# Kernel tuning notes

Hardware: AMD Instinct MI355X
Metric: run time of the kernel (lower is better)

The kernel has to match this reference:

```python
import jax, jax.numpy as jnp
import numpy as np

N_NODES = 100000
N_EDGES = 1600000
D_IN = 256
D_OUT = 256


def setup_inputs() -> dict:
    key = jax.random.key(0)
    k1, k2, k3, k4, k5 = jax.random.split(key, 5)
    x = jax.random.normal(k1, (N_NODES, D_IN), dtype=jnp.float32)
    edge_src = jax.random.randint(k2, (N_EDGES,), 0, N_NODES, dtype=jnp.int32)
    edge_dst = jax.random.randint(k3, (N_EDGES,), 0, N_NODES, dtype=jnp.int32)
    edge_val = jax.random.uniform(k4, (N_EDGES,), dtype=jnp.float32)
    stdv = 1.0 / np.sqrt(D_OUT)
    weight = jax.random.uniform(k5, (D_IN, D_OUT), dtype=jnp.float32,
                                minval=-stdv, maxval=stdv)
    return {"x": x, "edge_src": edge_src, "edge_dst": edge_dst,
            "edge_val": edge_val, "weight": weight}


def reference(x, edge_src, edge_dst, edge_val, weight):
    # torch.spmm(adj, x): out[dst] += adj_val * x[src]
    msgs = x[edge_src] * edge_val[:, None]                     # [E, D_IN]
    agg = jax.ops.segment_sum(msgs, edge_dst,
                              num_segments=x.shape[0])         # [N, D_IN]
    # torch.mm(aggregated, weight)
    return agg @ weight                                        # [N, D_OUT]
```

## Files before the change

kernel.cpp:

```cpp
#include <hip/hip_runtime.h>
#include <hip/hip_bf16.h>

#define D 256
#define BDST 128
#define CAP 3072
#define TILE 6144

typedef __attribute__((ext_vector_type(8))) short short8;
typedef __attribute__((ext_vector_type(4))) float f32x4;

static __device__ __forceinline__ unsigned short f2bf(float f) {
    union { float f; unsigned u; } u; u.f = f;
    unsigned r = u.u + 0x7FFF + ((u.u >> 16) & 1);
    return (unsigned short)(r >> 16);
}

static __device__ __forceinline__ float bf2f(unsigned short b) {
    union { unsigned u; float f; } u; u.u = ((unsigned)b) << 16;
    return u.f;
}

static __device__ __forceinline__ unsigned cvtpk(float a, float b) {
    unsigned r;
    asm("v_cvt_pk_bf16_f32 %0, %1, %2" : "=v"(r) : "v"(a), "v"(b));
    return r;
}

__global__ __launch_bounds__(64) void build_wf_kernel(
    const float* __restrict__ W, unsigned short* __restrict__ wF) {
    int fid = blockIdx.x;
    int kt = fid >> 4, nt = fid & 15;
    int lane = threadIdx.x;
    int col = nt * 16 + (lane & 15);
    int k0 = kt * 32 + (lane >> 4) * 8;
    unsigned short frag[8];
#pragma unroll
    for (int j = 0; j < 8; ++j) frag[j] = f2bf(W[(k0 + j) * D + col]);
    *(short8*)(wF + ((size_t)fid * 64 + lane) * 8) = *(short8*)frag;
}

__global__ __launch_bounds__(256) void gemm_kernel(
    const float* __restrict__ x, const unsigned short* __restrict__ wF,
    unsigned short* __restrict__ y, int n_nodes) {
    const int lane = threadIdx.x & 63;
    const int wave = threadIdx.x >> 6;
    const int rsel = lane & 15;
    const int koff = (lane >> 4) * 8;
    const int row0 = blockIdx.x * 64 + wave * 16;
    if (row0 >= n_nodes) return;

    int row = row0 + rsel;
    int rowc = row < n_nodes ? row : n_nodes - 1;
    const float* xp = x + (size_t)rowc * D + koff;

    short8 a[8];
#pragma unroll
    for (int kt = 0; kt < 8; ++kt) {
        f32x4 lo = *(const f32x4*)(xp + kt * 32);
        f32x4 hi = *(const f32x4*)(xp + kt * 32 + 4);
        union { unsigned u[4]; short8 s; } pk;
        pk.u[0] = cvtpk(lo[0], lo[1]);
        pk.u[1] = cvtpk(lo[2], lo[3]);
        pk.u[2] = cvtpk(hi[0], hi[1]);
        pk.u[3] = cvtpk(hi[2], hi[3]);
        a[kt] = pk.s;
    }

    f32x4 acc[16];
#pragma unroll
    for (int nt = 0; nt < 16; ++nt) acc[nt] = (f32x4){0.f, 0.f, 0.f, 0.f};

    const short8* wf = (const short8*)wF;
#pragma unroll
    for (int kt = 0; kt < 8; ++kt) {
#pragma unroll
        for (int nt = 0; nt < 16; ++nt) {
            short8 b = wf[(kt * 16 + nt) * 64 + lane];
            acc[nt] = __builtin_amdgcn_mfma_f32_16x16x32_bf16(a[kt], b, acc[nt], 0, 0, 0);
        }
    }

    int crow0 = row0 + (lane >> 4) * 4;
#pragma unroll
    for (int nt = 0; nt < 16; ++nt) {
        int ccol = nt * 16 + rsel;
#pragma unroll
        for (int i = 0; i < 4; ++i) {
            int r = crow0 + i;
            if (r < n_nodes) y[(size_t)r * D + ccol] = f2bf(acc[nt][i]);
        }
    }
}

__global__ __launch_bounds__(256) void hist_bucket_kernel(
    const int* __restrict__ edst, int* __restrict__ gcount,
    int n_edges, int nb) {
    __shared__ int h[1024];
    for (int j = threadIdx.x; j < nb; j += 256) h[j] = 0;
    __syncthreads();
    int i = blockIdx.x * 256 + threadIdx.x;
    int stride = gridDim.x * 256;
    for (; i < n_edges; i += stride) atomicAdd(&h[edst[i] >> 7], 1);
    __syncthreads();
    for (int j = threadIdx.x; j < nb; j += 256) {
        int v = h[j];
        if (v) atomicAdd(&gcount[j], v);
    }
}

__global__ __launch_bounds__(1024) void scan_bucket_kernel(
    const int* __restrict__ gcount, int* __restrict__ offs,
    int* __restrict__ cursor, int nb) {
    __shared__ int t[1024];
    int tid = threadIdx.x;
    int c = (tid < nb) ? gcount[tid] : 0;
    t[tid] = c;
    __syncthreads();
    for (int off = 1; off < 1024; off <<= 1) {
        int v = (tid >= off) ? t[tid - off] : 0;
        __syncthreads();
        t[tid] += v;
        __syncthreads();
    }
    if (tid < nb) { int e = t[tid] - c; offs[tid] = e; cursor[tid] = e; }
}

__global__ __launch_bounds__(1024) void fill_ms_kernel(
    const int* __restrict__ esrc, const int* __restrict__ edst,
    const float* __restrict__ eval, int* __restrict__ cursor,
    int2* __restrict__ binned, int n_edges, int nb) {
    __shared__ int lhist[1024];
    __shared__ int lscan[1024];
    __shared__ int lbase[1024];
    __shared__ int lcur[1024];

    int tid = threadIdx.x;
    int tb = blockIdx.x * TILE;
    int m = n_edges - tb; if (m > TILE) m = TILE;

    int src[6], dst[6]; float val[6];
#pragma unroll
    for (int j = 0; j < 6; ++j) {
        int i = tid + j * 1024;
        if (i < m) { src[j] = esrc[tb + i]; dst[j] = edst[tb + i]; val[j] = eval[tb + i]; }
    }

    for (int j = tid; j < nb; j += 1024) lhist[j] = 0;
    __syncthreads();
#pragma unroll
    for (int j = 0; j < 6; ++j)
        if (tid + j * 1024 < m) atomicAdd(&lhist[dst[j] >> 7], 1);
    __syncthreads();

    int c = (tid < nb) ? lhist[tid] : 0;
    lscan[tid] = c;
    __syncthreads();
    for (int off = 1; off < 1024; off <<= 1) {
        int v = (tid >= off) ? lscan[tid - off] : 0;
        __syncthreads();
        lscan[tid] += v;
        __syncthreads();
    }
    if (tid < nb) {
        int lofs = lscan[tid] - c;
        int gbase = c ? atomicAdd(&cursor[tid], c) : 0;
        lbase[tid] = gbase - lofs;
        lcur[tid] = lofs;
    }
    __syncthreads();

#pragma unroll
    for (int j = 0; j < 6; ++j) {
        if (tid + j * 1024 < m) {
            int d = dst[j];
            int b = d >> 7;
            int pos = atomicAdd(&lcur[b], 1);
            binned[lbase[b] + pos] =
                make_int2(src[j] | ((d & (BDST - 1)) << 20), __float_as_int(val[j]));
        }
    }
}

__global__ __launch_bounds__(512) void bucket_gather_kernel(
    const unsigned short* __restrict__ y, const int* __restrict__ offs,
    const int* __restrict__ bend, const int2* __restrict__ binned,
    float* __restrict__ out, int n_nodes) {
    __shared__ int2 lcsr[CAP];
    __shared__ int lhist[BDST];
    __shared__ int lscan[BDST];
    __shared__ int lofs[BDST];
    __shared__ int lcur[BDST];

    int b = blockIdx.x;
    int tid = threadIdx.x;
    int beg = offs[b];
    int end = bend[b];
    int cnt = end - beg;
    int nch = cnt > 0 ? (cnt + CAP - 1) / CAP : 1;

    const int hw = tid >> 5;
    const int lane = tid & 31;
    const unsigned short* yl = y + lane * 8;

    for (int c = 0; c < nch; ++c) {
        int cb = beg + c * CAP;
        int ce = cb + CAP < end ? cb + CAP : end;
        int m = ce > cb ? ce - cb : 0;

        int2 ec[6];
#pragma unroll
        for (int j = 0; j < 6; ++j) {
            int i = tid + j * 512;
            if (i < m) ec[j] = binned[cb + i];
        }

        for (int j = tid; j < BDST; j += 512) lhist[j] = 0;
        __syncthreads();
#pragma unroll
        for (int j = 0; j < 6; ++j)
            if (tid + j * 512 < m) atomicAdd(&lhist[(ec[j].x >> 20) & (BDST - 1)], 1);
        __syncthreads();
        if (tid < BDST) lscan[tid] = lhist[tid];
        __syncthreads();
        for (int off = 1; off < BDST; off <<= 1) {
            int v = 0;
            if (tid < BDST && tid >= off) v = lscan[tid - off];
            __syncthreads();
            if (tid < BDST) lscan[tid] += v;
            __syncthreads();
        }
        if (tid < BDST) {
            int e = lscan[tid] - lhist[tid];
            lofs[tid] = e;
            lcur[tid] = e;
        }
        __syncthreads();
#pragma unroll
        for (int j = 0; j < 6; ++j) {
            if (tid + j * 512 < m) {
                int pos = atomicAdd(&lcur[(ec[j].x >> 20) & (BDST - 1)], 1);
                lcsr[pos] = ec[j];
            }
        }
        __syncthreads();

        for (int dl = hw; dl < BDST; dl += 16) {
            int d = b * BDST + dl;
            if (d >= n_nodes) break;
            int i0 = lofs[dl];
            int i1 = lcur[dl];
            float acc[8] = {0.f, 0.f, 0.f, 0.f, 0.f, 0.f, 0.f, 0.f};
            int i = i0;
            for (; i + 4 <= i1; i += 4) {
                int2 e0 = lcsr[i];
                int2 e1 = lcsr[i + 1];
                int2 e2 = lcsr[i + 2];
                int2 e3 = lcsr[i + 3];
                short8 r0 = *(const short8*)(yl + (size_t)(e0.x & 0xFFFFF) * D);
                short8 r1 = *(const short8*)(yl + (size_t)(e1.x & 0xFFFFF) * D);
                short8 r2 = *(const short8*)(yl + (size_t)(e2.x & 0xFFFFF) * D);
                short8 r3 = *(const short8*)(yl + (size_t)(e3.x & 0xFFFFF) * D);
                float v0 = __int_as_float(e0.y), v1 = __int_as_float(e1.y);
                float v2 = __int_as_float(e2.y), v3 = __int_as_float(e3.y);
#pragma unroll
                for (int j = 0; j < 8; ++j) {
                    acc[j] += v0 * bf2f((unsigned short)r0[j]);
                    acc[j] += v1 * bf2f((unsigned short)r1[j]);
                    acc[j] += v2 * bf2f((unsigned short)r2[j]);
                    acc[j] += v3 * bf2f((unsigned short)r3[j]);
                }
            }
            for (; i < i1; ++i) {
                int2 e0 = lcsr[i];
                float v0 = __int_as_float(e0.y);
                short8 r0 = *(const short8*)(yl + (size_t)(e0.x & 0xFFFFF) * D);
#pragma unroll
                for (int j = 0; j < 8; ++j) acc[j] += v0 * bf2f((unsigned short)r0[j]);
            }
            float* op = out + (size_t)d * D + lane * 8;
            if (c == 0) {
                *(f32x4*)(op)     = (f32x4){acc[0], acc[1], acc[2], acc[3]};
                *(f32x4*)(op + 4) = (f32x4){acc[4], acc[5], acc[6], acc[7]};
            } else {
                f32x4 o0 = *(f32x4*)(op);
                f32x4 o1 = *(f32x4*)(op + 4);
                o0[0] += acc[0]; o0[1] += acc[1]; o0[2] += acc[2]; o0[3] += acc[3];
                o1[0] += acc[4]; o1[1] += acc[5]; o1[2] += acc[6]; o1[3] += acc[7];
                *(f32x4*)(op)     = o0;
                *(f32x4*)(op + 4) = o1;
            }
        }
        __syncthreads();
    }
}

extern "C" void kernel_launch(void* const* d_in, const int* in_sizes, int n_in,
                              void* d_out, int out_size, void* d_ws, size_t ws_size,
                              hipStream_t stream) {
    const float* x    = (const float*)d_in[0];
    const int*   esrc = (const int*)d_in[1];
    const int*   edst = (const int*)d_in[2];
    const float* eval = (const float*)d_in[3];
    const float* W    = (const float*)d_in[4];
    float* out = (float*)d_out;

    const int n_nodes = in_sizes[0] / D;
    const int n_edges = in_sizes[1];
    const int nb = (n_nodes + BDST - 1) / BDST;

    char* ws = (char*)d_ws;
    unsigned short* y  = (unsigned short*)ws;  ws += (size_t)n_nodes * D * 2;
    unsigned short* wF = (unsigned short*)ws;  ws += (size_t)D * D * 2;
    int*  gcount  = (int*)ws;                  ws += 4096;
    int*  offs    = (int*)ws;                  ws += 4096;
    int*  cursor  = (int*)ws;                  ws += 4096;
    int2* binned  = (int2*)ws;                 ws += (size_t)n_edges * 8;

    hipMemsetAsync(gcount, 0, (size_t)nb * sizeof(int), stream);

    build_wf_kernel<<<128, 64, 0, stream>>>(W, wF);
    gemm_kernel<<<(n_nodes + 63) / 64, 256, 0, stream>>>(x, wF, y, n_nodes);

    hist_bucket_kernel<<<256, 256, 0, stream>>>(edst, gcount, n_edges, nb);
    scan_bucket_kernel<<<1, 1024, 0, stream>>>(gcount, offs, cursor, nb);

    const int ntiles = (n_edges + TILE - 1) / TILE;
    fill_ms_kernel<<<ntiles, 1024, 0, stream>>>(esrc, edst, eval, cursor, binned, n_edges, nb);

    bucket_gather_kernel<<<nb, 512, 0, stream>>>(y, offs, cursor, binned, out, n_nodes);
}
```

Measured before the change: 244.5 us.

## Merge GEMM with edge binning and weight prep with histogram into shared launches

The weight fragment build is folded into the edge histogram kernel, and the dense GEMM is merged with the edge binning fill kernel. Block-index ranges pick the role, so the memory-bound binning and the MFMA GEMM can run at the same time on the GPU, with fewer launches. The fill tile shrinks to 256-thread blocks, each thread scanning 4 buckets. The gather kernel moves to 256 threads with a smaller per-chunk edge capacity. The costs are more global cursor atomics from the smaller fill tiles and fewer waves per gather block.

```diff
diff --git a/kernel.cpp b/kernel.cpp
--- a/kernel.cpp
+++ b/kernel.cpp
@@ -3,8 +3,8 @@
 
 #define D 256
 #define BDST 128
-#define CAP 3072
-#define TILE 6144
+#define CAP 2560
+#define TILE 2048
 
 typedef __attribute__((ext_vector_type(8))) short short8;
 typedef __attribute__((ext_vector_type(4))) float f32x4;
@@ -26,85 +26,33 @@
     return r;
 }
 
-__global__ __launch_bounds__(64) void build_wf_kernel(
-    const float* __restrict__ W, unsigned short* __restrict__ wF) {
-    int fid = blockIdx.x;
-    int kt = fid >> 4, nt = fid & 15;
-    int lane = threadIdx.x;
-    int col = nt * 16 + (lane & 15);
-    int k0 = kt * 32 + (lane >> 4) * 8;
-    unsigned short frag[8];
-#pragma unroll
-    for (int j = 0; j < 8; ++j) frag[j] = f2bf(W[(k0 + j) * D + col]);
-    *(short8*)(wF + ((size_t)fid * 64 + lane) * 8) = *(short8*)frag;
-}
-
-__global__ __launch_bounds__(256) void gemm_kernel(
-    const float* __restrict__ x, const unsigned short* __restrict__ wF,
-    unsigned short* __restrict__ y, int n_nodes) {
-    const int lane = threadIdx.x & 63;
-    const int wave = threadIdx.x >> 6;
-    const int rsel = lane & 15;
-    const int koff = (lane >> 4) * 8;
-    const int row0 = blockIdx.x * 64 + wave * 16;
-    if (row0 >= n_nodes) return;
-
-    int row = row0 + rsel;
-    int rowc = row < n_nodes ? row : n_nodes - 1;
-    const float* xp = x + (size_t)rowc * D + koff;
-
-    short8 a[8];
-#pragma unroll
-    for (int kt = 0; kt < 8; ++kt) {
-        f32x4 lo = *(const f32x4*)(xp + kt * 32);
-        f32x4 hi = *(const f32x4*)(xp + kt * 32 + 4);
-        union { unsigned u[4]; short8 s; } pk;
-        pk.u[0] = cvtpk(lo[0], lo[1]);
-        pk.u[1] = cvtpk(lo[2], lo[3]);
-        pk.u[2] = cvtpk(hi[0], hi[1]);
-        pk.u[3] = cvtpk(hi[2], hi[3]);
-        a[kt] = pk.s;
-    }
-
-    f32x4 acc[16];
-#pragma unroll
-    for (int nt = 0; nt < 16; ++nt) acc[nt] = (f32x4){0.f, 0.f, 0.f, 0.f};
-
-    const short8* wf = (const short8*)wF;
-#pragma unroll
-    for (int kt = 0; kt < 8; ++kt) {
-#pragma unroll
-        for (int nt = 0; nt < 16; ++nt) {
-            short8 b = wf[(kt * 16 + nt) * 64 + lane];
-            acc[nt] = __builtin_amdgcn_mfma_f32_16x16x32_bf16(a[kt], b, acc[nt], 0, 0, 0);
-        }
-    }
-
-    int crow0 = row0 + (lane >> 4) * 4;
-#pragma unroll
-    for (int nt = 0; nt < 16; ++nt) {
-        int ccol = nt * 16 + rsel;
-#pragma unroll
-        for (int i = 0; i < 4; ++i) {
-            int r = crow0 + i;
-            if (r < n_nodes) y[(size_t)r * D + ccol] = f2bf(acc[nt][i]);
-        }
-    }
-}
-
-__global__ __launch_bounds__(256) void hist_bucket_kernel(
+__global__ __launch_bounds__(256) void prep_kernel(
+    const float* __restrict__ W, unsigned short* __restrict__ wF,
     const int* __restrict__ edst, int* __restrict__ gcount,
     int n_edges, int nb) {
-    __shared__ int h[1024];
-    for (int j = threadIdx.x; j < nb; j += 256) h[j] = 0;
-    __syncthreads();
-    int i = blockIdx.x * 256 + threadIdx.x;
-    int stride = gridDim.x * 256;
-    for (; i < n_edges; i += stride) atomicAdd(&h[edst[i] >> 7], 1);
-    __syncthreads();
-    for (int j = threadIdx.x; j < nb; j += 256) {
-        int v = h[j];
-        if (v) atomicAdd(&gcount[j], v);
+    int tid = threadIdx.x;
+    if (blockIdx.x < 32) {
+        int fid = blockIdx.x * 4 + (tid >> 6);
+        int lane = tid & 63;
+        int kt = fid >> 4, nt = fid & 15;
+        int col = nt * 16 + (lane & 15);
+        int k0 = kt * 32 + (lane >> 4) * 8;
+        unsigned short frag[8];
+#pragma unroll
+        for (int j = 0; j < 8; ++j) frag[j] = f2bf(W[(k0 + j) * D + col]);
+        *(short8*)(wF + ((size_t)fid * 64 + lane) * 8) = *(short8*)frag;
+    } else {
+        __shared__ int h[1024];
+        for (int j = tid; j < nb; j += 256) h[j] = 0;
+        __syncthreads();
+        int i = (blockIdx.x - 32) * 256 + tid;
+        int stride = (gridDim.x - 32) * 256;
+        for (; i < n_edges; i += stride) atomicAdd(&h[edst[i] >> 7], 1);
+        __syncthreads();
+        for (int j = tid; j < nb; j += 256) {
+            int v = h[j];
+            if (v) atomicAdd(&gcount[j], v);
+        }
     }
 }
 
@@ -125,63 +73,126 @@
     if (tid < nb) { int e = t[tid] - c; offs[tid] = e; cursor[tid] = e; }
 }
 
-__global__ __launch_bounds__(1024) void fill_ms_kernel(
+__global__ __launch_bounds__(256) void gemm_fill_kernel(
+    const float* __restrict__ x, const unsigned short* __restrict__ wF,
+    unsigned short* __restrict__ y, int n_nodes,
     const int* __restrict__ esrc, const int* __restrict__ edst,
     const float* __restrict__ eval, int* __restrict__ cursor,
-    int2* __restrict__ binned, int n_edges, int nb) {
+    int2* __restrict__ binned, int n_edges, int nb, int nfill) {
     __shared__ int lhist[1024];
-    __shared__ int lscan[1024];
     __shared__ int lbase[1024];
     __shared__ int lcur[1024];
+    __shared__ int t[256];
 
     int tid = threadIdx.x;
-    int tb = blockIdx.x * TILE;
-    int m = n_edges - tb; if (m > TILE) m = TILE;
-
-    int src[6], dst[6]; float val[6];
-#pragma unroll
-    for (int j = 0; j < 6; ++j) {
-        int i = tid + j * 1024;
-        if (i < m) { src[j] = esrc[tb + i]; dst[j] = edst[tb + i]; val[j] = eval[tb + i]; }
+
+    if ((int)blockIdx.x < nfill) {
+        int tb = blockIdx.x * TILE;
+        int m = n_edges - tb; if (m > TILE) m = TILE;
+
+        int src[8], dst[8]; float val[8];
+#pragma unroll
+        for (int j = 0; j < 8; ++j) {
+            int i = tid + j * 256;
+            if (i < m) { src[j] = esrc[tb + i]; dst[j] = edst[tb + i]; val[j] = eval[tb + i]; }
+        }
+
+        for (int j = tid; j < 1024; j += 256) lhist[j] = 0;
+        __syncthreads();
+#pragma unroll
+        for (int j = 0; j < 8; ++j)
+            if (tid + j * 256 < m) atomicAdd(&lhist[dst[j] >> 7], 1);
+        __syncthreads();
+
+        int b0 = 4 * tid;
+        int c[4]; int s = 0;
+#pragma unroll
+        for (int q = 0; q < 4; ++q) { c[q] = lhist[b0 + q]; s += c[q]; }
+        t[tid] = s;
+        __syncthreads();
+        for (int off = 1; off < 256; off <<= 1) {
+            int v = (tid >= off) ? t[tid - off] : 0;
+            __syncthreads();
+            t[tid] += v;
+            __syncthreads();
+        }
+        int run = t[tid] - s;
+#pragma unroll
+        for (int q = 0; q < 4; ++q) {
+            int b = b0 + q;
+            if (b < nb && c[q]) {
+                int g = atomicAdd(&cursor[b], c[q]);
+                lbase[b] = g - run;
+            }
+            lcur[b] = run;
+            run += c[q];
+        }
+        __syncthreads();
+
+#pragma unroll
+        for (int j = 0; j < 8; ++j) {
+            if (tid + j * 256 < m) {
+                int d = dst[j];
+                int b = d >> 7;
+                int pos = atomicAdd(&lcur[b], 1);
+                binned[lbase[b] + pos] =
+                    make_int2(src[j] | ((d & (BDST - 1)) << 20), __float_as_int(val[j]));
+            }
+        }
+    } else {
+        int gbid = blockIdx.x - nfill;
+        const int lane = tid & 63;
+        const int wave = tid >> 6;
+        const int rsel = lane & 15;
+        const int koff = (lane >> 4) * 8;
+        const int row0 = gbid * 64 + wave * 16;
+        if (row0 >= n_nodes) return;
+
+        int row = row0 + rsel;
+        int rowc = row < n_nodes ? row : n_nodes - 1;
+        const float* xp = x + (size_t)rowc * D + koff;
+
+        short8 a[8];
+#pragma unroll
+        for (int kt = 0; kt < 8; ++kt) {
+            f32x4 lo = *(const f32x4*)(xp + kt * 32);
+            f32x4 hi = *(const f32x4*)(xp + kt * 32 + 4);
+            union { unsigned u[4]; short8 s; } pk;
+            pk.u[0] = cvtpk(lo[0], lo[1]);
+            pk.u[1] = cvtpk(lo[2], lo[3]);
+            pk.u[2] = cvtpk(hi[0], hi[1]);
+            pk.u[3] = cvtpk(hi[2], hi[3]);
+            a[kt] = pk.s;
+        }
+
+        f32x4 acc[16];
+#pragma unroll
+        for (int nt = 0; nt < 16; ++nt) acc[nt] = (f32x4){0.f, 0.f, 0.f, 0.f};
+
+        const short8* wf = (const short8*)wF;
+#pragma unroll
+        for (int kt = 0; kt < 8; ++kt) {
+#pragma unroll
+            for (int nt = 0; nt < 16; ++nt) {
+                short8 b = wf[(kt * 16 + nt) * 64 + lane];
+                acc[nt] = __builtin_amdgcn_mfma_f32_16x16x32_bf16(a[kt], b, acc[nt], 0, 0, 0);
+            }
+        }
+
+        int crow0 = row0 + (lane >> 4) * 4;
+#pragma unroll
+        for (int nt = 0; nt < 16; ++nt) {
+            int ccol = nt * 16 + rsel;
+#pragma unroll
+            for (int i = 0; i < 4; ++i) {
+                int r = crow0 + i;
+                if (r < n_nodes) y[(size_t)r * D + ccol] = f2bf(acc[nt][i]);
+            }
+        }
     }
-
-    for (int j = tid; j < nb; j += 1024) lhist[j] = 0;
-    __syncthreads();
-#pragma unroll
-    for (int j = 0; j < 6; ++j)
-        if (tid + j * 1024 < m) atomicAdd(&lhist[dst[j] >> 7], 1);
-    __syncthreads();
-
-    int c = (tid < nb) ? lhist[tid] : 0;
-    lscan[tid] = c;
-    __syncthreads();
-    for (int off = 1; off < 1024; off <<= 1) {
-        int v = (tid >= off) ? lscan[tid - off] : 0;
-        __syncthreads();
-        lscan[tid] += v;
-        __syncthreads();
-    }
-    if (tid < nb) {
-        int lofs = lscan[tid] - c;
-        int gbase = c ? atomicAdd(&cursor[tid], c) : 0;
-        lbase[tid] = gbase - lofs;
-        lcur[tid] = lofs;
-    }
-    __syncthreads();
-
-#pragma unroll
-    for (int j = 0; j < 6; ++j) {
-        if (tid + j * 1024 < m) {
-            int d = dst[j];
-            int b = d >> 7;
-            int pos = atomicAdd(&lcur[b], 1);
-            binned[lbase[b] + pos] =
-                make_int2(src[j] | ((d & (BDST - 1)) << 20), __float_as_int(val[j]));
-        }
-    }
-}
-
-__global__ __launch_bounds__(512) void bucket_gather_kernel(
+}
+
+__global__ __launch_bounds__(256) void bucket_gather_kernel(
     const unsigned short* __restrict__ y, const int* __restrict__ offs,
     const int* __restrict__ bend, const int2* __restrict__ binned,
     float* __restrict__ out, int n_nodes) {
@@ -207,18 +218,18 @@
         int ce = cb + CAP < end ? cb + CAP : end;
         int m = ce > cb ? ce - cb : 0;
 
-        int2 ec[6];
-#pragma unroll
-        for (int j = 0; j < 6; ++j) {
-            int i = tid + j * 512;
+        int2 ec[10];
+#pragma unroll
+        for (int j = 0; j < 10; ++j) {
+            int i = tid + j * 256;
             if (i < m) ec[j] = binned[cb + i];
         }
 
-        for (int j = tid; j < BDST; j += 512) lhist[j] = 0;
-        __syncthreads();
-#pragma unroll
-        for (int j = 0; j < 6; ++j)
-            if (tid + j * 512 < m) atomicAdd(&lhist[(ec[j].x >> 20) & (BDST - 1)], 1);
+        if (tid < BDST) lhist[tid] = 0;
+        __syncthreads();
+#pragma unroll
+        for (int j = 0; j < 10; ++j)
+            if (tid + j * 256 < m) atomicAdd(&lhist[(ec[j].x >> 20) & (BDST - 1)], 1);
         __syncthreads();
         if (tid < BDST) lscan[tid] = lhist[tid];
         __syncthreads();
@@ -236,15 +247,15 @@
         }
         __syncthreads();
 #pragma unroll
-        for (int j = 0; j < 6; ++j) {
-            if (tid + j * 512 < m) {
+        for (int j = 0; j < 10; ++j) {
+            if (tid + j * 256 < m) {
                 int pos = atomicAdd(&lcur[(ec[j].x >> 20) & (BDST - 1)], 1);
                 lcsr[pos] = ec[j];
             }
         }
         __syncthreads();
 
-        for (int dl = hw; dl < BDST; dl += 16) {
+        for (int dl = hw; dl < BDST; dl += 8) {
             int d = b * BDST + dl;
             if (d >= n_nodes) break;
             int i0 = lofs[dl];
@@ -318,14 +329,14 @@
 
     hipMemsetAsync(gcount, 0, (size_t)nb * sizeof(int), stream);
 
-    build_wf_kernel<<<128, 64, 0, stream>>>(W, wF);
-    gemm_kernel<<<(n_nodes + 63) / 64, 256, 0, stream>>>(x, wF, y, n_nodes);
-
-    hist_bucket_kernel<<<256, 256, 0, stream>>>(edst, gcount, n_edges, nb);
+    prep_kernel<<<256, 256, 0, stream>>>(W, wF, edst, gcount, n_edges, nb);
+
     scan_bucket_kernel<<<1, 1024, 0, stream>>>(gcount, offs, cursor, nb);
 
-    const int ntiles = (n_edges + TILE - 1) / TILE;
-    fill_ms_kernel<<<ntiles, 1024, 0, stream>>>(esrc, edst, eval, cursor, binned, n_edges, nb);
-
-    bucket_gather_kernel<<<nb, 512, 0, stream>>>(y, offs, cursor, binned, out, n_nodes);
-}
+    const int nfill = (n_edges + TILE - 1) / TILE;
+    const int ngemm = (n_nodes + 63) / 64;
+    gemm_fill_kernel<<<nfill + ngemm, 256, 0, stream>>>(
+        x, wF, y, n_nodes, esrc, edst, eval, cursor, binned, n_edges, nb, nfill);
+
+    bucket_gather_kernel<<<nb, 256, 0, stream>>>(y, offs, cursor, binned, out, n_nodes);
+}
```

After: 300.1 us. +22.7%, slower.
